# Kernel optimization log

Hardware: AMD Instinct MI355X
Metric: run time of the kernel (lower is better)

## Reference

```python
import jax, jax.numpy as jnp
from jax import lax
import numpy as np

B, T, I, H, O = 512, 2048, 8, 128, 96


def setup_inputs() -> dict:
    key = jax.random.key(0)
    ks = jax.random.split(key, 7)
    s = 1.0 / np.sqrt(H)  # PyTorch GRU init scale
    return {
        "x": jax.random.normal(ks[0], (B, T, I), dtype=jnp.float32),
        "w_ih": jax.random.uniform(ks[1], (3 * H, I), jnp.float32, -s, s),
        "w_hh": jax.random.uniform(ks[2], (3 * H, H), jnp.float32, -s, s),
        "b_ih": jax.random.uniform(ks[3], (3 * H,), jnp.float32, -s, s),
        "b_hh": jax.random.uniform(ks[4], (3 * H,), jnp.float32, -s, s),
        "fc_w": jax.random.uniform(ks[5], (O, H), jnp.float32, -s, s),
        "fc_b": jax.random.uniform(ks[6], (O,), jnp.float32, -s, s),
    }


def reference(x, w_ih, w_hh, b_ih, b_hh, fc_w, fc_b):
    # x: [B, T, I]; PyTorch GRU gate order: reset, update, new (r, z, n)
    Bh, Th, _ = x.shape
    Hh = w_hh.shape[1]
    # Precompute input contributions for all timesteps in one big GEMM.
    gx_all = jnp.einsum('bti,gi->btg', x, w_ih) + b_ih      # [B, T, 3H]
    gx_all = jnp.swapaxes(gx_all, 0, 1)                     # [T, B, 3H]

    def step(h, gx):
        gh = h @ w_hh.T + b_hh                              # [B, 3H]
        r = jax.nn.sigmoid(gx[:, :Hh] + gh[:, :Hh])
        z = jax.nn.sigmoid(gx[:, Hh:2 * Hh] + gh[:, Hh:2 * Hh])
        n = jnp.tanh(gx[:, 2 * Hh:] + r * gh[:, 2 * Hh:])
        h_new = (1.0 - z) * n + z * h
        return h_new, None

    h0 = jnp.zeros((Bh, Hh), x.dtype)
    h_last, _ = lax.scan(step, h0, gx_all)                  # h at final timestep
    return h_last @ fc_w.T + fc_b                           # [B, O]
```

## Files before the change

kernel.cpp:

```cpp
#include <hip/hip_runtime.h>

#define BB 512
#define TT 2048
#define II 8
#define HH 128
#define OO 96

typedef __attribute__((ext_vector_type(8))) short bf16x8;
typedef __attribute__((ext_vector_type(4))) float f32x4;

__device__ __forceinline__ float fast_rcp(float x) { return __builtin_amdgcn_rcpf(x); }
__device__ __forceinline__ float sigmoid_fast(float x) { return fast_rcp(1.0f + __expf(-x)); }
__device__ __forceinline__ float tanh_fast(float x) {
    return 1.0f - 2.0f * fast_rcp(1.0f + __expf(2.0f * x));
}
__device__ __forceinline__ unsigned short f2bf(float f) {
    unsigned int u = __builtin_bit_cast(unsigned int, f);
    u += 0x7fffu + ((u >> 16) & 1u);
    return (unsigned short)(u >> 16);
}
__device__ __forceinline__ float bf2f(unsigned short h) {
    unsigned int u = ((unsigned int)h) << 16;
    return __builtin_bit_cast(float, u);
}

__device__ __forceinline__ float dot8(const float w[8], float4 a, float4 b, float acc) {
    acc = fmaf(w[0], a.x, acc); acc = fmaf(w[1], a.y, acc);
    acc = fmaf(w[2], a.z, acc); acc = fmaf(w[3], a.w, acc);
    acc = fmaf(w[4], b.x, acc); acc = fmaf(w[5], b.y, acc);
    acc = fmaf(w[6], b.z, acc); acc = fmaf(w[7], b.w, acc);
    return acc;
}

__global__ __launch_bounds__(512, 2) void gru_kernel(
    const float* __restrict__ x,
    const float* __restrict__ w_ih,
    const float* __restrict__ w_hh,
    const float* __restrict__ b_ih,
    const float* __restrict__ b_hh,
    const float* __restrict__ fc_w,
    const float* __restrict__ fc_b,
    float* __restrict__ out)
{
    __shared__ __align__(16) char hbuf[2 * 1280];
    __shared__ __align__(16) float hfin[2][HH];

    const int tid = threadIdx.x;
    const int wv  = tid >> 6;
    const int ln  = tid & 63;
    const int col = ln & 15;
    const int g4  = ln >> 4;
    const int b   = g4 & 1;
    const int p   = ((ln >> 2) & 1) * 2 + (ln & 1);
    const int j   = 16 * wv + col;
    const int b0  = blockIdx.x * 2;

    auto ldfrag_hh = [&](int grow, int ks) {
        const float* rowp = w_hh + grow * HH + 32 * ks + g4 * 8;
        float4 u = *(const float4*)(rowp);
        float4 v = *(const float4*)(rowp + 4);
        bf16x8 f;
        f[0] = (short)f2bf(u.x); f[1] = (short)f2bf(u.y);
        f[2] = (short)f2bf(u.z); f[3] = (short)f2bf(u.w);
        f[4] = (short)f2bf(v.x); f[5] = (short)f2bf(v.y);
        f[6] = (short)f2bf(v.z); f[7] = (short)f2bf(v.w);
        return f;
    };

    bf16x8 bR[4], bZ[4], bN[4];
#pragma unroll
    for (int ks = 0; ks < 4; ++ks) {
        bR[ks] = ldfrag_hh(j, ks);
        bZ[ks] = ldfrag_hh(HH + j, ks);
        bN[ks] = ldfrag_hh(2 * HH + j, ks);
    }

    float wr[8], wz[8], wn[8];
    {
        float4 u, v;
        u = *(const float4*)(w_ih + j * II);            v = *(const float4*)(w_ih + j * II + 4);
        wr[0]=u.x; wr[1]=u.y; wr[2]=u.z; wr[3]=u.w; wr[4]=v.x; wr[5]=v.y; wr[6]=v.z; wr[7]=v.w;
        u = *(const float4*)(w_ih + (HH + j) * II);     v = *(const float4*)(w_ih + (HH + j) * II + 4);
        wz[0]=u.x; wz[1]=u.y; wz[2]=u.z; wz[3]=u.w; wz[4]=v.x; wz[5]=v.y; wz[6]=v.z; wz[7]=v.w;
        u = *(const float4*)(w_ih + (2 * HH + j) * II); v = *(const float4*)(w_ih + (2 * HH + j) * II + 4);
        wn[0]=u.x; wn[1]=u.y; wn[2]=u.z; wn[3]=u.w; wn[4]=v.x; wn[5]=v.y; wn[6]=v.z; wn[7]=v.w;
    }

    const float bias_r  = b_ih[j] + b_hh[j];
    const float bias_z  = b_ih[HH + j] + b_hh[HH + j];
    const float bias_nh = b_hh[2 * HH + j];
    const float bias_nx = b_ih[2 * HH + j];

    for (int i = tid; i < 640; i += 512) ((int*)hbuf)[i] = 0;
    __syncthreads();

    const char* abase = hbuf + p * 320 + g4 * 16;
    char* wbase = hbuf + b * 640 + (j << 1);
    const float* xp = x + (size_t)(b0 + b) * TT * II;

    float h0 = 0.f;
    const f32x4 zf = {0.f, 0.f, 0.f, 0.f};

    float gxr0, gxz0, gxn0, gxr1, gxz1, gxn1;
    {
        float4 xa = *(const float4*)(xp);          float4 xb = *(const float4*)(xp + 4);
        float4 xc = *(const float4*)(xp + II);     float4 xd = *(const float4*)(xp + II + 4);
        gxr0 = dot8(wr, xa, xb, bias_r);
        gxz0 = dot8(wz, xa, xb, bias_z);
        gxn0 = dot8(wn, xa, xb, bias_nx);
        gxr1 = dot8(wr, xc, xd, bias_r);
        gxz1 = dot8(wz, xc, xd, bias_z);
        gxn1 = dot8(wn, xc, xd, bias_nx);
    }

#define STEP(RBUF, GXR, GXZ, GXN)                                               \
    {                                                                           \
        const char* ab = abase + (RBUF) * 1280;                                 \
        bf16x8 a0 = *(const bf16x8*)(ab);                                       \
        bf16x8 a1 = *(const bf16x8*)(ab + 64);                                  \
        bf16x8 a2 = *(const bf16x8*)(ab + 128);                                 \
        bf16x8 a3 = *(const bf16x8*)(ab + 192);                                 \
        f32x4 aR = zf, aZ = zf, aN = zf;                                        \
        aR = __builtin_amdgcn_mfma_f32_16x16x32_bf16(a0, bR[0], aR, 0, 0, 0);   \
        aZ = __builtin_amdgcn_mfma_f32_16x16x32_bf16(a0, bZ[0], aZ, 0, 0, 0);   \
        aN = __builtin_amdgcn_mfma_f32_16x16x32_bf16(a0, bN[0], aN, 0, 0, 0);   \
        aR = __builtin_amdgcn_mfma_f32_16x16x32_bf16(a1, bR[1], aR, 0, 0, 0);   \
        aZ = __builtin_amdgcn_mfma_f32_16x16x32_bf16(a1, bZ[1], aZ, 0, 0, 0);   \
        aN = __builtin_amdgcn_mfma_f32_16x16x32_bf16(a1, bN[1], aN, 0, 0, 0);   \
        aR = __builtin_amdgcn_mfma_f32_16x16x32_bf16(a2, bR[2], aR, 0, 0, 0);   \
        aZ = __builtin_amdgcn_mfma_f32_16x16x32_bf16(a2, bZ[2], aZ, 0, 0, 0);   \
        aN = __builtin_amdgcn_mfma_f32_16x16x32_bf16(a2, bN[2], aN, 0, 0, 0);   \
        aR = __builtin_amdgcn_mfma_f32_16x16x32_bf16(a3, bR[3], aR, 0, 0, 0);   \
        aZ = __builtin_amdgcn_mfma_f32_16x16x32_bf16(a3, bZ[3], aZ, 0, 0, 0);   \
        aN = __builtin_amdgcn_mfma_f32_16x16x32_bf16(a3, bN[3], aN, 0, 0, 0);   \
        float gr = aR[0] + aR[1] + (GXR);                                       \
        float gz = aZ[0] + aZ[1] + (GXZ);                                       \
        float gn = aN[0] + aN[1] + bias_nh;                                     \
        float r0 = sigmoid_fast(gr);                                            \
        float z0 = sigmoid_fast(gz);                                            \
        float n0 = tanh_fast(fmaf(r0, gn, (GXN)));                              \
        h0 = fmaf(z0, h0 - n0, n0);                                             \
        if (ln < 32) {                                                          \
            char* w_ = wbase + (1 - (RBUF)) * 1280;                             \
            unsigned short s0 = f2bf(h0);                                       \
            *(unsigned short*)(w_)       = s0;                                  \
            *(unsigned short*)(w_ + 320) = f2bf(h0 - bf2f(s0));                 \
        }                                                                       \
        __syncthreads();                                                        \
    }

    for (int it = 0; it < TT / 2; ++it) {
        int t2 = 2 * it + 2; if (t2 > TT - 1) t2 = TT - 1;
        int t3 = 2 * it + 3; if (t3 > TT - 1) t3 = TT - 1;
        float4 pa = *(const float4*)(xp + t2 * II);
        float4 pb = *(const float4*)(xp + t2 * II + 4);
        float4 pc = *(const float4*)(xp + t3 * II);
        float4 pd = *(const float4*)(xp + t3 * II + 4);

        STEP(0, gxr0, gxz0, gxn0)
        STEP(1, gxr1, gxz1, gxn1)

        gxr0 = dot8(wr, pa, pb, bias_r);
        gxz0 = dot8(wz, pa, pb, bias_z);
        gxn0 = dot8(wn, pa, pb, bias_nx);
        gxr1 = dot8(wr, pc, pd, bias_r);
        gxz1 = dot8(wz, pc, pd, bias_z);
        gxn1 = dot8(wn, pc, pd, bias_nx);
    }
#undef STEP

    if (ln < 32) hfin[b][j] = h0;
    __syncthreads();

    if (tid < 2 * OO) {
        const int bb2 = (tid >= OO) ? 1 : 0;
        const int o   = tid - OO * bb2;
        const float4* hf = (const float4*)(&hfin[bb2][0]);
        const float4* wp = (const float4*)(fc_w + o * HH);
        float acc = fc_b[o];
#pragma unroll 8
        for (int v = 0; v < HH / 4; ++v) {
            float4 w4 = wp[v];
            float4 h4 = hf[v];
            acc = fmaf(w4.x, h4.x, acc); acc = fmaf(w4.y, h4.y, acc);
            acc = fmaf(w4.z, h4.z, acc); acc = fmaf(w4.w, h4.w, acc);
        }
        out[(size_t)(b0 + bb2) * OO + o] = acc;
    }
}

extern "C" void kernel_launch(void* const* d_in, const int* in_sizes, int n_in,
                              void* d_out, int out_size, void* d_ws, size_t ws_size,
                              hipStream_t stream) {
    const float* x    = (const float*)d_in[0];
    const float* w_ih = (const float*)d_in[1];
    const float* w_hh = (const float*)d_in[2];
    const float* b_ih = (const float*)d_in[3];
    const float* b_hh = (const float*)d_in[4];
    const float* fc_w = (const float*)d_in[5];
    const float* fc_b = (const float*)d_in[6];
    float* out = (float*)d_out;

    gru_kernel<<<BB / 2, 512, 0, stream>>>(x, w_ih, w_hh, b_ih, b_hh, fc_w, fc_b, out);
}
```

Baseline: 996.9 us.

## Halve block to 4 waves with 32 columns per wave and prescaled exp2 gates

Each block now runs 4 wavefronts instead of 8, and each wave computes two 16-column tiles, so it issues 24 MFMAs per step. All lanes do useful gate work by selecting tile A or B, where before half the lanes sat idle. Weights and biases are prescaled by ±log2(e) so the activations use exp2 directly, and the gx term is seeded into the MFMA accumulator. The input dot products are interleaved inside the second step to hide MFMA latency. The aim is cheaper barriers and better lane use, at the cost of more registers and a longer serial MFMA chain per wave.

Result: slower. 1.105 ms (+10.8%).

```diff
diff --git a/kernel.cpp b/kernel.cpp
--- a/kernel.cpp
+++ b/kernel.cpp
@@ -9,10 +9,15 @@
 typedef __attribute__((ext_vector_type(8))) short bf16x8;
 typedef __attribute__((ext_vector_type(4))) float f32x4;
 
+#define L2E 1.4426950408889634f
+
 __device__ __forceinline__ float fast_rcp(float x) { return __builtin_amdgcn_rcpf(x); }
-__device__ __forceinline__ float sigmoid_fast(float x) { return fast_rcp(1.0f + __expf(-x)); }
-__device__ __forceinline__ float tanh_fast(float x) {
-    return 1.0f - 2.0f * fast_rcp(1.0f + __expf(2.0f * x));
+__device__ __forceinline__ float exp2_fast(float x) {
+#if __has_builtin(__builtin_amdgcn_exp2f)
+    return __builtin_amdgcn_exp2f(x);
+#else
+    return __expf(x * 0.6931471805599453f);
+#endif
 }
 __device__ __forceinline__ unsigned short f2bf(float f) {
     unsigned int u = __builtin_bit_cast(unsigned int, f);
@@ -23,7 +28,6 @@
     unsigned int u = ((unsigned int)h) << 16;
     return __builtin_bit_cast(float, u);
 }
-
 __device__ __forceinline__ float dot8(const float w[8], float4 a, float4 b, float acc) {
     acc = fmaf(w[0], a.x, acc); acc = fmaf(w[1], a.y, acc);
     acc = fmaf(w[2], a.z, acc); acc = fmaf(w[3], a.w, acc);
@@ -32,7 +36,7 @@
     return acc;
 }
 
-__global__ __launch_bounds__(512, 2) void gru_kernel(
+__global__ __launch_bounds__(256, 1) void gru_kernel(
     const float* __restrict__ x,
     const float* __restrict__ w_ih,
     const float* __restrict__ w_hh,
@@ -51,96 +55,125 @@
     const int col = ln & 15;
     const int g4  = ln >> 4;
     const int b   = g4 & 1;
+    const int sel = g4 >> 1;
     const int p   = ((ln >> 2) & 1) * 2 + (ln & 1);
-    const int j   = 16 * wv + col;
+    const int jA  = 32 * wv + col;
+    const int jB  = jA + 16;
+    const int jS  = jA + 16 * sel;
     const int b0  = blockIdx.x * 2;
 
-    auto ldfrag_hh = [&](int grow, int ks) {
+    auto ldfrag_hh = [&](int grow, int ks, float sc) {
         const float* rowp = w_hh + grow * HH + 32 * ks + g4 * 8;
         float4 u = *(const float4*)(rowp);
         float4 v = *(const float4*)(rowp + 4);
         bf16x8 f;
-        f[0] = (short)f2bf(u.x); f[1] = (short)f2bf(u.y);
-        f[2] = (short)f2bf(u.z); f[3] = (short)f2bf(u.w);
-        f[4] = (short)f2bf(v.x); f[5] = (short)f2bf(v.y);
-        f[6] = (short)f2bf(v.z); f[7] = (short)f2bf(v.w);
+        f[0] = (short)f2bf(sc * u.x); f[1] = (short)f2bf(sc * u.y);
+        f[2] = (short)f2bf(sc * u.z); f[3] = (short)f2bf(sc * u.w);
+        f[4] = (short)f2bf(sc * v.x); f[5] = (short)f2bf(sc * v.y);
+        f[6] = (short)f2bf(sc * v.z); f[7] = (short)f2bf(sc * v.w);
         return f;
     };
 
-    bf16x8 bR[4], bZ[4], bN[4];
+    bf16x8 bRA[4], bZA[4], bNA[4], bRB[4], bZB[4], bNB[4];
 #pragma unroll
     for (int ks = 0; ks < 4; ++ks) {
-        bR[ks] = ldfrag_hh(j, ks);
-        bZ[ks] = ldfrag_hh(HH + j, ks);
-        bN[ks] = ldfrag_hh(2 * HH + j, ks);
+        bRA[ks] = ldfrag_hh(jA, ks, -L2E);
+        bZA[ks] = ldfrag_hh(HH + jA, ks, -L2E);
+        bNA[ks] = ldfrag_hh(2 * HH + jA, ks, 2.0f * L2E);
+        bRB[ks] = ldfrag_hh(jB, ks, -L2E);
+        bZB[ks] = ldfrag_hh(HH + jB, ks, -L2E);
+        bNB[ks] = ldfrag_hh(2 * HH + jB, ks, 2.0f * L2E);
     }
 
     float wr[8], wz[8], wn[8];
     {
-        float4 u, v;
-        u = *(const float4*)(w_ih + j * II);            v = *(const float4*)(w_ih + j * II + 4);
-        wr[0]=u.x; wr[1]=u.y; wr[2]=u.z; wr[3]=u.w; wr[4]=v.x; wr[5]=v.y; wr[6]=v.z; wr[7]=v.w;
-        u = *(const float4*)(w_ih + (HH + j) * II);     v = *(const float4*)(w_ih + (HH + j) * II + 4);
-        wz[0]=u.x; wz[1]=u.y; wz[2]=u.z; wz[3]=u.w; wz[4]=v.x; wz[5]=v.y; wz[6]=v.z; wz[7]=v.w;
-        u = *(const float4*)(w_ih + (2 * HH + j) * II); v = *(const float4*)(w_ih + (2 * HH + j) * II + 4);
-        wn[0]=u.x; wn[1]=u.y; wn[2]=u.z; wn[3]=u.w; wn[4]=v.x; wn[5]=v.y; wn[6]=v.z; wn[7]=v.w;
-    }
-
-    const float bias_r  = b_ih[j] + b_hh[j];
-    const float bias_z  = b_ih[HH + j] + b_hh[HH + j];
-    const float bias_nh = b_hh[2 * HH + j];
-    const float bias_nx = b_ih[2 * HH + j];
-
-    for (int i = tid; i < 640; i += 512) ((int*)hbuf)[i] = 0;
+        const float* r0p = w_ih + jS * II;
+        const float* r1p = w_ih + (HH + jS) * II;
+        const float* r2p = w_ih + (2 * HH + jS) * II;
+#pragma unroll
+        for (int i = 0; i < 8; ++i) {
+            wr[i] = -L2E * r0p[i];
+            wz[i] = -L2E * r1p[i];
+            wn[i] = (2.0f * L2E) * r2p[i];
+        }
+    }
+
+    const float bias_r2  = -L2E * (b_ih[jS] + b_hh[jS]);
+    const float bias_z2  = -L2E * (b_ih[HH + jS] + b_hh[HH + jS]);
+    const float bias_nh2 = (2.0f * L2E) * b_hh[2 * HH + jS];
+    const float bias_nx2 = (2.0f * L2E) * b_ih[2 * HH + jS];
+
+    for (int i = tid; i < 640; i += 256) ((int*)hbuf)[i] = 0;
     __syncthreads();
 
     const char* abase = hbuf + p * 320 + g4 * 16;
-    char* wbase = hbuf + b * 640 + (j << 1);
+    char* wbase = hbuf + b * 640 + (jS << 1);
     const float* xp = x + (size_t)(b0 + b) * TT * II;
 
     float h0 = 0.f;
-    const f32x4 zf = {0.f, 0.f, 0.f, 0.f};
 
     float gxr0, gxz0, gxn0, gxr1, gxz1, gxn1;
     {
         float4 xa = *(const float4*)(xp);          float4 xb = *(const float4*)(xp + 4);
         float4 xc = *(const float4*)(xp + II);     float4 xd = *(const float4*)(xp + II + 4);
-        gxr0 = dot8(wr, xa, xb, bias_r);
-        gxz0 = dot8(wz, xa, xb, bias_z);
-        gxn0 = dot8(wn, xa, xb, bias_nx);
-        gxr1 = dot8(wr, xc, xd, bias_r);
-        gxz1 = dot8(wz, xc, xd, bias_z);
-        gxn1 = dot8(wn, xc, xd, bias_nx);
-    }
-
-#define STEP(RBUF, GXR, GXZ, GXN)                                               \
+        gxr0 = dot8(wr, xa, xb, bias_r2);  gxz0 = dot8(wz, xa, xb, bias_z2);  gxn0 = dot8(wn, xa, xb, bias_nx2);
+        gxr1 = dot8(wr, xc, xd, bias_r2);  gxz1 = dot8(wz, xc, xd, bias_z2);  gxn1 = dot8(wn, xc, xd, bias_nx2);
+    }
+    float gxr0n, gxz0n, gxn0n, gxr1n, gxz1n, gxn1n;
+
+#define MFMA_BF16 __builtin_amdgcn_mfma_f32_16x16x32_bf16
+
+#define STEP(RBUF, GXR, GXZ, GXN, DOTS)                                         \
     {                                                                           \
         const char* ab = abase + (RBUF) * 1280;                                 \
         bf16x8 a0 = *(const bf16x8*)(ab);                                       \
         bf16x8 a1 = *(const bf16x8*)(ab + 64);                                  \
         bf16x8 a2 = *(const bf16x8*)(ab + 128);                                 \
         bf16x8 a3 = *(const bf16x8*)(ab + 192);                                 \
-        f32x4 aR = zf, aZ = zf, aN = zf;                                        \
-        aR = __builtin_amdgcn_mfma_f32_16x16x32_bf16(a0, bR[0], aR, 0, 0, 0);   \
-        aZ = __builtin_amdgcn_mfma_f32_16x16x32_bf16(a0, bZ[0], aZ, 0, 0, 0);   \
-        aN = __builtin_amdgcn_mfma_f32_16x16x32_bf16(a0, bN[0], aN, 0, 0, 0);   \
-        aR = __builtin_amdgcn_mfma_f32_16x16x32_bf16(a1, bR[1], aR, 0, 0, 0);   \
-        aZ = __builtin_amdgcn_mfma_f32_16x16x32_bf16(a1, bZ[1], aZ, 0, 0, 0);   \
-        aN = __builtin_amdgcn_mfma_f32_16x16x32_bf16(a1, bN[1], aN, 0, 0, 0);   \
-        aR = __builtin_amdgcn_mfma_f32_16x16x32_bf16(a2, bR[2], aR, 0, 0, 0);   \
-        aZ = __builtin_amdgcn_mfma_f32_16x16x32_bf16(a2, bZ[2], aZ, 0, 0, 0);   \
-        aN = __builtin_amdgcn_mfma_f32_16x16x32_bf16(a2, bN[2], aN, 0, 0, 0);   \
-        aR = __builtin_amdgcn_mfma_f32_16x16x32_bf16(a3, bR[3], aR, 0, 0, 0);   \
-        aZ = __builtin_amdgcn_mfma_f32_16x16x32_bf16(a3, bZ[3], aZ, 0, 0, 0);   \
-        aN = __builtin_amdgcn_mfma_f32_16x16x32_bf16(a3, bN[3], aN, 0, 0, 0);   \
-        float gr = aR[0] + aR[1] + (GXR);                                       \
-        float gz = aZ[0] + aZ[1] + (GXZ);                                       \
-        float gn = aN[0] + aN[1] + bias_nh;                                     \
-        float r0 = sigmoid_fast(gr);                                            \
-        float z0 = sigmoid_fast(gz);                                            \
-        float n0 = tanh_fast(fmaf(r0, gn, (GXN)));                              \
+        f32x4 aRA = {(GXR), 0.f, 0.f, 0.f};                                     \
+        f32x4 aZA = {(GXZ), 0.f, 0.f, 0.f};                                     \
+        f32x4 aNA = {bias_nh2, 0.f, 0.f, 0.f};                                  \
+        f32x4 aRB = {(GXR), 0.f, 0.f, 0.f};                                     \
+        f32x4 aZB = {(GXZ), 0.f, 0.f, 0.f};                                     \
+        f32x4 aNB = {bias_nh2, 0.f, 0.f, 0.f};                                  \
+        float gxn_ = (GXN);                                                     \
+        aRA = MFMA_BF16(a0, bRA[0], aRA, 0, 0, 0);                              \
+        aZA = MFMA_BF16(a0, bZA[0], aZA, 0, 0, 0);                              \
+        aNA = MFMA_BF16(a0, bNA[0], aNA, 0, 0, 0);                              \
+        aRB = MFMA_BF16(a0, bRB[0], aRB, 0, 0, 0);                              \
+        aZB = MFMA_BF16(a0, bZB[0], aZB, 0, 0, 0);                              \
+        aNB = MFMA_BF16(a0, bNB[0], aNB, 0, 0, 0);                              \
+        aRA = MFMA_BF16(a1, bRA[1], aRA, 0, 0, 0);                              \
+        aZA = MFMA_BF16(a1, bZA[1], aZA, 0, 0, 0);                              \
+        aNA = MFMA_BF16(a1, bNA[1], aNA, 0, 0, 0);                              \
+        aRB = MFMA_BF16(a1, bRB[1], aRB, 0, 0, 0);                              \
+        aZB = MFMA_BF16(a1, bZB[1], aZB, 0, 0, 0);                              \
+        aNB = MFMA_BF16(a1, bNB[1], aNB, 0, 0, 0);                              \
+        aRA = MFMA_BF16(a2, bRA[2], aRA, 0, 0, 0);                              \
+        aZA = MFMA_BF16(a2, bZA[2], aZA, 0, 0, 0);                              \
+        aNA = MFMA_BF16(a2, bNA[2], aNA, 0, 0, 0);                              \
+        aRB = MFMA_BF16(a2, bRB[2], aRB, 0, 0, 0);                              \
+        aZB = MFMA_BF16(a2, bZB[2], aZB, 0, 0, 0);                              \
+        aNB = MFMA_BF16(a2, bNB[2], aNB, 0, 0, 0);                              \
+        aRA = MFMA_BF16(a3, bRA[3], aRA, 0, 0, 0);                              \
+        aZA = MFMA_BF16(a3, bZA[3], aZA, 0, 0, 0);                              \
+        aNA = MFMA_BF16(a3, bNA[3], aNA, 0, 0, 0);                              \
+        aRB = MFMA_BF16(a3, bRB[3], aRB, 0, 0, 0);                              \
+        aZB = MFMA_BF16(a3, bZB[3], aZB, 0, 0, 0);                              \
+        aNB = MFMA_BF16(a3, bNB[3], aNB, 0, 0, 0);                              \
+        DOTS                                                                    \
+        float grA = aRA[0] + aRA[1], grB = aRB[0] + aRB[1];                     \
+        float gzA = aZA[0] + aZA[1], gzB = aZB[0] + aZB[1];                     \
+        float gnA = aNA[0] + aNA[1], gnB = aNB[0] + aNB[1];                     \
+        float gr = sel ? grB : grA;                                             \
+        float gz = sel ? gzB : gzA;                                             \
+        float gn = sel ? gnB : gnA;                                             \
+        float r0 = fast_rcp(1.0f + exp2_fast(gr));                              \
+        float z0 = fast_rcp(1.0f + exp2_fast(gz));                              \
+        float t0 = fast_rcp(1.0f + exp2_fast(fmaf(r0, gn, gxn_)));              \
+        float n0 = fmaf(-2.0f, t0, 1.0f);                                       \
         h0 = fmaf(z0, h0 - n0, n0);                                             \
-        if (ln < 32) {                                                          \
+        {                                                                       \
             char* w_ = wbase + (1 - (RBUF)) * 1280;                             \
             unsigned short s0 = f2bf(h0);                                       \
             *(unsigned short*)(w_)       = s0;                                  \
@@ -151,25 +184,28 @@
 
     for (int it = 0; it < TT / 2; ++it) {
         int t2 = 2 * it + 2; if (t2 > TT - 1) t2 = TT - 1;
-        int t3 = 2 * it + 3; if (t3 > TT - 1) t3 = TT - 1;
-        float4 pa = *(const float4*)(xp + t2 * II);
-        float4 pb = *(const float4*)(xp + t2 * II + 4);
-        float4 pc = *(const float4*)(xp + t3 * II);
-        float4 pd = *(const float4*)(xp + t3 * II + 4);
-
-        STEP(0, gxr0, gxz0, gxn0)
-        STEP(1, gxr1, gxz1, gxn1)
-
-        gxr0 = dot8(wr, pa, pb, bias_r);
-        gxz0 = dot8(wz, pa, pb, bias_z);
-        gxn0 = dot8(wn, pa, pb, bias_nx);
-        gxr1 = dot8(wr, pc, pd, bias_r);
-        gxz1 = dot8(wz, pc, pd, bias_z);
-        gxn1 = dot8(wn, pc, pd, bias_nx);
+        int t3 = t2 + 1;     if (t3 > TT - 1) t3 = TT - 1;
+        float4 pa = *(const float4*)(xp + (size_t)t2 * II);
+        float4 pb = *(const float4*)(xp + (size_t)t2 * II + 4);
+        float4 pc = *(const float4*)(xp + (size_t)t3 * II);
+        float4 pd = *(const float4*)(xp + (size_t)t3 * II + 4);
+
+        STEP(0, gxr0, gxz0, gxn0, {})
+        STEP(1, gxr1, gxz1, gxn1, {
+            gxr0n = dot8(wr, pa, pb, bias_r2);
+            gxz0n = dot8(wz, pa, pb, bias_z2);
+            gxn0n = dot8(wn, pa, pb, bias_nx2);
+            gxr1n = dot8(wr, pc, pd, bias_r2);
+            gxz1n = dot8(wz, pc, pd, bias_z2);
+            gxn1n = dot8(wn, pc, pd, bias_nx2);
+        })
+        gxr0 = gxr0n; gxz0 = gxz0n; gxn0 = gxn0n;
+        gxr1 = gxr1n; gxz1 = gxz1n; gxn1 = gxn1n;
     }
 #undef STEP
-
-    if (ln < 32) hfin[b][j] = h0;
+#undef MFMA_BF16
+
+    hfin[b][jS] = h0;
     __syncthreads();
 
     if (tid < 2 * OO) {
@@ -201,5 +237,5 @@
     const float* fc_b = (const float*)d_in[6];
     float* out = (float*)d_out;
 
-    gru_kernel<<<BB / 2, 512, 0, stream>>>(x, w_ih, w_hh, b_ih, b_hh, fc_w, fc_b, out);
-}
+    gru_kernel<<<BB / 2, 256, 0, stream>>>(x, w_ih, w_hh, b_ih, b_hh, fc_w, fc_b, out);
+}
```
